# Kernel optimization log

Hardware: AMD Instinct MI355X
Metric: run time of the kernel (lower is better)

Reference implementation:

```python
import jax, jax.numpy as jnp
import numpy as np

H, D, Kd, Vd = 16, 1024, 64, 64
N, Mlen = 4096, 4096


def setup_inputs() -> dict:
    key = jax.random.key(0)
    ks = jax.random.split(key, 7)
    X = jax.random.normal(ks[0], (N, D), dtype=jnp.float32)
    M = jax.random.normal(ks[1], (Mlen, D), dtype=jnp.float32)
    mask = jax.random.randint(ks[2], (N, Mlen), 0, 2, dtype=jnp.int32)
    Wq = jax.random.normal(ks[3], (H, D, Kd), dtype=jnp.float32)
    Wk = jax.random.normal(ks[4], (H, D, Kd), dtype=jnp.float32)
    Wv = jax.random.normal(ks[5], (H, D, Vd), dtype=jnp.float32)
    Wo = jax.random.normal(ks[6], (H, Vd, D), dtype=jnp.float32)
    return {"X": X, "M": M, "mask": mask, "Wq": Wq, "Wk": Wk, "Wv": Wv, "Wo": Wo}


def reference(X, M, mask, Wq, Wk, Wv, Wo):
    # Projections: [h,n,k], [h,m,k], [h,m,v]
    Q = jnp.einsum('nd,hdk->hnk', X, Wq)
    K = jnp.einsum('md,hdk->hmk', M, Wk)
    V = jnp.einsum('md,hdv->hmv', M, Wv)
    # Masked attention (no scaling, matching the source)
    logits = jnp.einsum('hnk,hmk->hnm', Q, K)
    logits = jnp.where(mask[None, :, :] == 0, -jnp.inf, logits)
    weights = jax.nn.softmax(logits, axis=-1)
    O = jnp.einsum('hnm,hmv->hnv', weights, V)
    Y = jnp.einsum('hnv,hvd->nd', O, Wo)
    return Y
```

## Files before the change

kernel.cpp:

```cpp
#include <hip/hip_runtime.h>

typedef _Float16 half8 __attribute__((ext_vector_type(8)));
typedef _Float16 half4 __attribute__((ext_vector_type(4)));
typedef __fp16 fp16x2 __attribute__((ext_vector_type(2)));
typedef short short8 __attribute__((ext_vector_type(8)));
typedef short short4v __attribute__((ext_vector_type(4)));
typedef float floatx4 __attribute__((ext_vector_type(4)));

#define LOG2E 1.4426950408889634f

#define GLDS16(g, l) __builtin_amdgcn_global_load_lds( \
    (const __attribute__((address_space(1))) unsigned int*)(g), \
    (__attribute__((address_space(3))) unsigned int*)(l), 16, 0, 0)

static __device__ __forceinline__ short f2bf(float f){
  union { float f; unsigned u; } v; v.f = f;
  unsigned r = v.u + 0x7fffu + ((v.u >> 16) & 1u);
  return (short)(r >> 16);
}
static __device__ __forceinline__ float bf2f(short s){
  union { unsigned u; float f; } v; v.u = ((unsigned)(unsigned short)s) << 16;
  return v.f;
}

__global__ __launch_bounds__(256) void kconvA(const float* __restrict__ X,
                                              const float* __restrict__ Mm,
                                              short* __restrict__ XFh, short* __restrict__ XFl,
                                              short* __restrict__ MFh, short* __restrict__ MFl){
  int b = blockIdx.x;
  int t = threadIdx.x, w = t >> 6, l = t & 63, quad = l >> 4;
  int srcsel = b >> 8, ntile = b & 255;
  const float* A = srcsel ? Mm : X;
  short* oh = srcsel ? MFh : XFh;
  short* ol = srcsel ? MFl : XFl;
  int row = ntile*16 + (l & 15);
  #pragma unroll
  for (int i = 0; i < 8; i++){
    int kt = w*8 + i;
    const float* p = A + (size_t)row*1024 + kt*32 + quad*8;
    float4 v0 = *(const float4*)p, v1 = *(const float4*)(p + 4);
    float vv[8] = {v0.x,v0.y,v0.z,v0.w,v1.x,v1.y,v1.z,v1.w};
    short8 hh, ll;
    #pragma unroll
    for (int j = 0; j < 8; j++){
      short hb = f2bf(vv[j]); hh[j] = hb; ll[j] = f2bf(vv[j] - bf2f(hb));
    }
    size_t off = ((size_t)kt*256 + ntile)*512 + l*8;
    *(short8*)&oh[off] = hh;
    *(short8*)&ol[off] = ll;
  }
}

__global__ __launch_bounds__(256) void kconvW2(const float* __restrict__ Wq,
                                               const float* __restrict__ Wk,
                                               const float* __restrict__ Wv,
                                               short* __restrict__ WFh, short* __restrict__ WFl){
  __shared__ float T[128][68];
  int bidx = blockIdx.x, g = blockIdx.y;
  int mat = bidx >> 4, h = bidx & 15;
  const float* W = (mat == 0 ? Wq : (mat == 1 ? Wk : Wv)) + (size_t)h*65536;
  int t = threadIdx.x, w = t >> 6, l = t & 63, quad = (l >> 4) & 3, fl = l & 15;
  #pragma unroll
  for (int p = 0; p < 32; p++){
    int idx = p*256 + t, row = idx >> 6, col = idx & 63;
    T[row][col] = W[(size_t)(g*128 + row)*64 + col];
  }
  __syncthreads();
  for (int ktl = 0; ktl < 4; ktl++){
    short8 hh, ll;
    #pragma unroll
    for (int j = 0; j < 8; j++){
      float v = T[ktl*32 + quad*8 + j][w*16 + fl];
      short hb = f2bf(v); hh[j] = hb; ll[j] = f2bf(v - bf2f(hb));
    }
    size_t frag = ((size_t)bidx*32 + g*4 + ktl)*4 + w;
    *(short8*)&WFh[frag*512 + l*8] = hh;
    *(short8*)&WFl[frag*512 + l*8] = ll;
  }
}

__global__ __launch_bounds__(256) void kmaskpack(const int* __restrict__ mask,
                                                 unsigned* __restrict__ bits){
  int w = blockIdx.x * 256 + threadIdx.x;
  const int* p = mask + (size_t)w * 32;
  unsigned b = 0;
  #pragma unroll
  for (int i = 0; i < 32; i++) b |= (p[i] != 0) ? (1u << i) : 0u;
  bits[w] = b;
}

__global__ __launch_bounds__(256) void ktransw(const float* __restrict__ src,
                                               short* __restrict__ dsth,
                                               short* __restrict__ dstl,
                                               int R, int C){
  __shared__ float tile[32][33];
  size_t boff = (size_t)blockIdx.z * R * C;
  src += boff; dsth += boff; dstl += boff;
  int r0 = blockIdx.y*32, c0 = blockIdx.x*32;
  int t = threadIdx.x, tr = t >> 3, tc = (t & 7)*4;
  const float* s = src + (size_t)(r0 + tr)*C + c0 + tc;
  #pragma unroll
  for (int i = 0; i < 4; i++) tile[tr][tc + i] = s[i];
  __syncthreads();
  short* dh = dsth + (size_t)(c0 + tr)*R + r0 + tc;
  short* dl = dstl + (size_t)(c0 + tr)*R + r0 + tc;
  #pragma unroll
  for (int i = 0; i < 4; i++){
    float v = tile[tc + i][tr];
    short hb = f2bf(v);
    dh[i] = hb; dl[i] = f2bf(v - bf2f(hb));
  }
}

__global__ __launch_bounds__(256,2) void kproj2(
    const short* __restrict__ XFh, const short* __restrict__ XFl,
    const short* __restrict__ MFh, const short* __restrict__ MFl,
    const short* __restrict__ WFh, const short* __restrict__ WFl,
    _Float16* __restrict__ QFh, _Float16* __restrict__ QFl,
    _Float16* __restrict__ KFh, _Float16* __restrict__ KFl,
    _Float16* __restrict__ VF)
{
  __shared__ short AhL[4096], AlL[4096], BhL[2048], BlL[2048];
  int cb = blockIdx.x, rb = blockIdx.y;
  int mat = cb >> 4, h = cb & 15;
  const short* Ah = (mat == 0) ? XFh : MFh;
  const short* Al = (mat == 0) ? XFl : MFl;
  int t = threadIdx.x, w = t >> 6, l = t & 63, quad = l >> 4, ln = l & 15;
  floatx4 acc[2][4] = {};
  for (int kt = 0; kt < 32; kt++){
    __syncthreads();
    size_t abase = ((size_t)kt*256 + rb*8)*512;
    #pragma unroll
    for (int i = 0; i < 2; i++){
      int cidx = i*256 + t;
      GLDS16(Ah + abase + cidx*8, &AhL[(i*256 + w*64)*8]);
      GLDS16(Al + abase + cidx*8, &AlL[(i*256 + w*64)*8]);
    }
    size_t bbase = (((size_t)cb*32 + kt)*4)*512;
    GLDS16(WFh + bbase + t*8, &BhL[(w*64)*8]);
    GLDS16(WFl + bbase + t*8, &BlL[(w*64)*8]);
    __syncthreads();
    short8 bh[4], bl[4];
    #pragma unroll
    for (int nt = 0; nt < 4; nt++){
      bh[nt] = *(short8*)&BhL[nt*512 + l*8];
      bl[nt] = *(short8*)&BlL[nt*512 + l*8];
    }
    #pragma unroll
    for (int mt = 0; mt < 2; mt++){
      short8 ah = *(short8*)&AhL[(w*2 + mt)*512 + l*8];
      short8 al = *(short8*)&AlL[(w*2 + mt)*512 + l*8];
      #pragma unroll
      for (int nt = 0; nt < 4; nt++){
        acc[mt][nt] = __builtin_amdgcn_mfma_f32_16x16x32_bf16(ah, bh[nt], acc[mt][nt], 0, 0, 0);
        acc[mt][nt] = __builtin_amdgcn_mfma_f32_16x16x32_bf16(ah, bl[nt], acc[mt][nt], 0, 0, 0);
        acc[mt][nt] = __builtin_amdgcn_mfma_f32_16x16x32_bf16(al, bh[nt], acc[mt][nt], 0, 0, 0);
      }
    }
  }
  int row0 = rb*128;
  if (mat == 2){
    #pragma unroll
    for (int mt = 0; mt < 2; mt++)
      #pragma unroll
      for (int nt = 0; nt < 4; nt++){
        union { fp16x2 h2[2]; unsigned u2[2]; } pu;
        pu.h2[0] = __builtin_amdgcn_cvt_pkrtz(acc[mt][nt][0], acc[mt][nt][1]);
        pu.h2[1] = __builtin_amdgcn_cvt_pkrtz(acc[mt][nt][2], acc[mt][nt][3]);
        size_t base = (((size_t)h*32 + rb)*16 + nt*4 + w)*512;
        *(uint2*)&VF[base + (quad*16 + ln)*8 + mt*4] = *(uint2*)&pu.u2[0];
      }
  } else {
    #pragma unroll
    for (int mt = 0; mt < 2; mt++)
      #pragma unroll
      for (int nt = 0; nt < 4; nt++)
        #pragma unroll
        for (int rg = 0; rg < 4; rg++){
          int n = row0 + w*32 + mt*16 + quad*4 + rg;
          int c = nt*16 + ln;
          float v = acc[mt][nt][rg];
          if (mat == 0) v *= LOG2E;
          _Float16 hi = (_Float16)v;
          _Float16 lo = (_Float16)(v - (float)hi);
          int lane2 = (n & 15) + (((c >> 3) & 3) << 4);
          size_t off = (((size_t)h*256 + (n >> 4))*2 + (c >> 5))*512 + lane2*8 + (c & 7);
          if (mat == 0){ QFh[off] = hi; QFl[off] = lo; }
          else         { KFh[off] = hi; KFl[off] = lo; }
        }
  }
}

__global__ __launch_bounds__(256,4) void kattn7(
    const _Float16* __restrict__ QFh, const _Float16* __restrict__ QFl,
    const _Float16* __restrict__ KFh, const _Float16* __restrict__ KFl,
    const _Float16* __restrict__ VF, const unsigned* __restrict__ bits,
    short* __restrict__ Ows)
{
  __shared__ _Float16 KBh[2][4096], KBl[2][4096], VB[4096];
  int bx = blockIdx.x, h = bx & 15, qb = bx >> 4, q0 = qb*64;
  int t = threadIdx.x, w = t >> 6, l = t & 63, quad = l >> 4, ln = l & 15;

  half8 qh[2], ql[2];
  #pragma unroll
  for (int kc = 0; kc < 2; kc++){
    size_t off = (((size_t)h*256 + qb*4 + w)*2 + kc)*512 + l*8;
    qh[kc] = *(const half8*)&QFh[off];
    ql[kc] = *(const half8*)&QFl[off];
  }

  floatx4 o[4] = {};
  float mst = -1e30f, lst = 0.f;

  const size_t hb = (size_t)h*262144;
  const int cidx0 = t, cidx1 = 256 + t;
  const int ld0 = (w*64)*8, ld1 = (256 + w*64)*8;

  {
    GLDS16(KFh + hb + cidx0*8, &KBh[0][ld0]);
    GLDS16(KFh + hb + cidx1*8, &KBh[0][ld1]);
    GLDS16(KFl + hb + cidx0*8, &KBl[0][ld0]);
    GLDS16(KFl + hb + cidx1*8, &KBl[0][ld1]);
    #pragma unroll
    for (int i = 0; i < 2; i++){
      int cidx = i*256 + t;
      int lu = cidx >> 6, uoff = (cidx & 63)*8;
      int gu = (lu >> 1)*4 + (lu & 1);
      GLDS16(VF + hb + (size_t)gu*512 + uoff, &VB[(i*256 + w*64)*8]);
    }
  }
  uint2 mwv = *(const uint2*)&bits[(size_t)(q0 + w*16 + ln)*128];
  __syncthreads();

  int cur = 0;
  for (int kt = 0; kt < 64; kt++){
    int ktn = (kt + 1) & 63;
    size_t kbn = hb + (size_t)ktn*4096;
    GLDS16(KFh + kbn + cidx0*8, &KBh[cur^1][ld0]);
    GLDS16(KFh + kbn + cidx1*8, &KBh[cur^1][ld1]);
    GLDS16(KFl + kbn + cidx0*8, &KBl[cur^1][ld0]);
    GLDS16(KFl + kbn + cidx1*8, &KBl[cur^1][ld1]);
    uint2 mwn = *(const uint2*)&bits[(size_t)(q0 + w*16 + ln)*128 + ktn*2];

    floatx4 st[4] = {};
    #pragma unroll
    for (int kc = 0; kc < 2; kc++)
      #pragma unroll
      for (int m8 = 0; m8 < 4; m8++){
        half8 kh = *(half8*)&KBh[cur][(m8*2 + kc)*512 + l*8];
        half8 kl = *(half8*)&KBl[cur][(m8*2 + kc)*512 + l*8];
        st[m8] = __builtin_amdgcn_mfma_f32_16x16x32_f16(kh, qh[kc], st[m8], 0, 0, 0);
        st[m8] = __builtin_amdgcn_mfma_f32_16x16x32_f16(kl, qh[kc], st[m8], 0, 0, 0);
        st[m8] = __builtin_amdgcn_mfma_f32_16x16x32_f16(kh, ql[kc], st[m8], 0, 0, 0);
      }

    {
      const unsigned mwp[2] = {mwv.x, mwv.y};
      #pragma unroll
      for (int m8 = 0; m8 < 4; m8++){
        unsigned nib = (mwp[m8 >> 1] >> ((m8 & 1)*16 + quad*4)) & 15u;
        #pragma unroll
        for (int rg = 0; rg < 4; rg++)
          if (!((nib >> rg) & 1u)) st[m8][rg] = -1e30f;
      }
      float a0 = fmaxf(fmaxf(st[0][0], st[0][1]), fmaxf(st[0][2], st[0][3]));
      float a1 = fmaxf(fmaxf(st[1][0], st[1][1]), fmaxf(st[1][2], st[1][3]));
      float a2 = fmaxf(fmaxf(st[2][0], st[2][1]), fmaxf(st[2][2], st[2][3]));
      float a3 = fmaxf(fmaxf(st[3][0], st[3][1]), fmaxf(st[3][2], st[3][3]));
      float mx = fmaxf(fmaxf(a0, a1), fmaxf(a2, a3));
      mx = fmaxf(mx, __shfl_xor(mx, 16));
      mx = fmaxf(mx, __shfl_xor(mx, 32));
      if (__any(mx > mst + 8.0f)){
        float mnew = fmaxf(mst, mx);
        float alpha = exp2f(mst - mnew);
        mst = mnew;
        lst *= alpha;
        #pragma unroll
        for (int vt = 0; vt < 4; vt++) o[vt] *= alpha;
      }
      float ssum = 0.f;
      #pragma unroll
      for (int m8 = 0; m8 < 4; m8++)
        #pragma unroll
        for (int rg = 0; rg < 4; rg++){
          float p = exp2f(st[m8][rg] - mst);
          st[m8][rg] = p; ssum += p;
        }
      ssum += __shfl_xor(ssum, 16);
      ssum += __shfl_xor(ssum, 32);
      lst += ssum;
    }
    mwv = mwn;

    __syncthreads();

    #pragma unroll
    for (int p = 0; p < 2; p++){
      half8 vfp[4];
      #pragma unroll
      for (int vt = 0; vt < 4; vt++)
        vfp[vt] = *(half8*)&VB[((vt*2 + p)*512) + l*8];
      #pragma unroll
      for (int sub = 0; sub < 2; sub++){
        int m8 = p*2 + sub;
        union { fp16x2 h2[2]; half4 h4; } pu;
        pu.h2[0] = __builtin_amdgcn_cvt_pkrtz(st[m8][0], st[m8][1]);
        pu.h2[1] = __builtin_amdgcn_cvt_pkrtz(st[m8][2], st[m8][3]);
        #pragma unroll
        for (int vt = 0; vt < 4; vt++){
          half4 va = sub ? __builtin_shufflevector(vfp[vt], vfp[vt], 4,5,6,7)
                         : __builtin_shufflevector(vfp[vt], vfp[vt], 0,1,2,3);
          o[vt] = __builtin_amdgcn_mfma_f32_16x16x16f16(va, pu.h4, o[vt], 0, 0, 0);
        }
      }
    }

    __syncthreads();

    {
      size_t vbn = hb + (size_t)(ktn >> 1)*8192;
      int vhalf = (ktn & 1)*2;
      #pragma unroll
      for (int i = 0; i < 2; i++){
        int cidx = i*256 + t;
        int lu = cidx >> 6, uoff = (cidx & 63)*8;
        int gu = (lu >> 1)*4 + vhalf + (lu & 1);
        GLDS16(VF + vbn + (size_t)gu*512 + uoff, &VB[(i*256 + w*64)*8]);
      }
    }
    cur ^= 1;
  }

  {
    float inv = (lst > 0.f) ? (1.f / lst) : 0.f;
    int n = q0 + w*16 + ln;
    #pragma unroll
    for (int vt = 0; vt < 4; vt++){
      short4v pk;
      #pragma unroll
      for (int rg = 0; rg < 4; rg++) pk[rg] = f2bf(o[vt][rg]*inv);
      *(short4v*)&Ows[(size_t)n*1024 + h*64 + vt*16 + quad*4] = pk;
    }
  }
}

__global__ __launch_bounds__(256,2) void kfinal(const short* __restrict__ Ain,
                                                const short* __restrict__ Bt,
                                                float* __restrict__ Y)
{
  __shared__ short Al[128*48];
  __shared__ short Bl[64*48];
  int cb = blockIdx.x, rb = blockIdx.y;
  int row0 = rb*128, col0 = cb*64;
  int t = threadIdx.x, w = t >> 6, l = t & 63, quad = l >> 4, ln = l & 15;
  floatx4 acc[2][4] = {};
  for (int d0 = 0; d0 < 1024; d0 += 32){
    #pragma unroll
    for (int i = 0; i < 2; i++){
      int u = t + i*256, r = u >> 2, s = u & 3;
      *(int4*)&Al[r*48 + s*8] = *(const int4*)&Ain[(size_t)(row0 + r)*1024 + d0 + s*8];
    }
    { int r = t >> 2, s = t & 3;
      *(int4*)&Bl[r*48 + s*8] = *(const int4*)&Bt[(size_t)(col0 + r)*1024 + d0 + s*8]; }
    __syncthreads();
    short8 bf[4];
    #pragma unroll
    for (int nt = 0; nt < 4; nt++) bf[nt] = *(short8*)&Bl[(nt*16 + ln)*48 + quad*8];
    #pragma unroll
    for (int mt = 0; mt < 2; mt++){
      short8 af = *(short8*)&Al[(w*32 + mt*16 + ln)*48 + quad*8];
      #pragma unroll
      for (int nt = 0; nt < 4; nt++)
        acc[mt][nt] = __builtin_amdgcn_mfma_f32_16x16x32_bf16(af, bf[nt], acc[mt][nt], 0, 0, 0);
    }
    __syncthreads();
  }
  #pragma unroll
  for (int mt = 0; mt < 2; mt++)
    #pragma unroll
    for (int nt = 0; nt < 4; nt++)
      #pragma unroll
      for (int rg = 0; rg < 4; rg++){
        int n = row0 + w*32 + mt*16 + quad*4 + rg;
        int c = col0 + nt*16 + ln;
        Y[(size_t)n*1024 + c] = acc[mt][nt][rg];
      }
}

extern "C" void kernel_launch(void* const* d_in, const int* in_sizes, int n_in,
                              void* d_out, int out_size, void* d_ws, size_t ws_size,
                              hipStream_t stream){
  (void)in_sizes; (void)n_in; (void)out_size; (void)ws_size;
  const float* X    = (const float*)d_in[0];
  const float* Mm   = (const float*)d_in[1];
  const int*   mask = (const int*)d_in[2];
  const float* Wq   = (const float*)d_in[3];
  const float* Wk   = (const float*)d_in[4];
  const float* Wv   = (const float*)d_in[5];
  const float* Wo   = (const float*)d_in[6];
  float* Y = (float*)d_out;
  char* ws = (char*)d_ws;
  const size_t MB = 1024*1024;
  short*    XFh   = (short*)   (ws +  0*MB);
  short*    XFl   = (short*)   (ws +  8*MB);
  short*    MFh   = (short*)   (ws + 16*MB);
  short*    MFl   = (short*)   (ws + 24*MB);
  short*    WFh   = (short*)   (ws + 32*MB);
  short*    WFl   = (short*)   (ws + 38*MB);
  unsigned* bits  = (unsigned*)(ws + 44*MB);
  _Float16* QFh   = (_Float16*)(ws + 46*MB);
  _Float16* QFl   = (_Float16*)(ws + 54*MB);
  _Float16* KFh   = (_Float16*)(ws + 62*MB);
  _Float16* KFl   = (_Float16*)(ws + 70*MB);
  _Float16* VF    = (_Float16*)(ws + 78*MB);
  short*    Ows   = (short*)   (ws +  0*MB);
  short*    Wot   = (short*)   (ws +  8*MB);
  short*    Wotl  = (short*)   (ws + 10*MB);

  kconvA<<<512, 256, 0, stream>>>(X, Mm, XFh, XFl, MFh, MFl);
  kconvW2<<<dim3(48,8), 256, 0, stream>>>(Wq, Wk, Wv, WFh, WFl);
  kmaskpack<<<2048, 256, 0, stream>>>(mask, bits);
  kproj2<<<dim3(48,32), 256, 0, stream>>>(XFh, XFl, MFh, MFl, WFh, WFl,
                                          QFh, QFl, KFh, KFl, VF);
  ktransw<<<dim3(32,32,1), 256, 0, stream>>>(Wo, Wot, Wotl, 1024, 1024);
  kattn7<<<1024, 256, 0, stream>>>(QFh, QFl, KFh, KFl, VF, bits, Ows);
  kfinal<<<dim3(16,32), 256, 0, stream>>>(Ows, Wot, Y);
}
```

Before: 489.2 us.

## Fuse K and V projections sharing M tiles; raise MFMA priority in attention

The projection kernel now computes K and V in one block, loading each M tile once and running two weight sets against it. The grid shrinks from 48 to 32 column blocks, and the occupancy hint changes from 2 to 3. The attention kernel wraps its MFMA phases in s_setprio to favour matrix issue across waves. It also defers the cross-lane reduction of the softmax denominator to the end of the loop instead of doing it every tile. The costs are more accumulator registers and LDS in the fused blocks, and uneven work between Q blocks and K/V blocks.

```diff
diff --git a/kernel.cpp b/kernel.cpp
--- a/kernel.cpp
+++ b/kernel.cpp
@@ -112,7 +112,7 @@
   }
 }
 
-__global__ __launch_bounds__(256,2) void kproj2(
+__global__ __launch_bounds__(256,3) void kproj3(
     const short* __restrict__ XFh, const short* __restrict__ XFl,
     const short* __restrict__ MFh, const short* __restrict__ MFl,
     const short* __restrict__ WFh, const short* __restrict__ WFl,
@@ -120,13 +120,14 @@
     _Float16* __restrict__ KFh, _Float16* __restrict__ KFl,
     _Float16* __restrict__ VF)
 {
-  __shared__ short AhL[4096], AlL[4096], BhL[2048], BlL[2048];
+  __shared__ short AhL[4096], AlL[4096], BhL[4096], BlL[4096];
   int cb = blockIdx.x, rb = blockIdx.y;
-  int mat = cb >> 4, h = cb & 15;
-  const short* Ah = (mat == 0) ? XFh : MFh;
-  const short* Al = (mat == 0) ? XFl : MFl;
+  const bool fused = (cb >= 16);
+  int h = fused ? (cb - 16) : cb;
+  const short* Ah = fused ? MFh : XFh;
+  const short* Al = fused ? MFl : XFl;
   int t = threadIdx.x, w = t >> 6, l = t & 63, quad = l >> 4, ln = l & 15;
-  floatx4 acc[2][4] = {};
+  floatx4 acc[2][8] = {};
   for (int kt = 0; kt < 32; kt++){
     __syncthreads();
     size_t abase = ((size_t)kt*256 + rb*8)*512;
@@ -136,40 +137,71 @@
       GLDS16(Ah + abase + cidx*8, &AhL[(i*256 + w*64)*8]);
       GLDS16(Al + abase + cidx*8, &AlL[(i*256 + w*64)*8]);
     }
-    size_t bbase = (((size_t)cb*32 + kt)*4)*512;
-    GLDS16(WFh + bbase + t*8, &BhL[(w*64)*8]);
-    GLDS16(WFl + bbase + t*8, &BlL[(w*64)*8]);
-    __syncthreads();
-    short8 bh[4], bl[4];
-    #pragma unroll
-    for (int nt = 0; nt < 4; nt++){
-      bh[nt] = *(short8*)&BhL[nt*512 + l*8];
-      bl[nt] = *(short8*)&BlL[nt*512 + l*8];
-    }
+    size_t bb0 = (((size_t)cb*32 + kt)*4)*512;
+    GLDS16(WFh + bb0 + t*8, &BhL[(w*64)*8]);
+    GLDS16(WFl + bb0 + t*8, &BlL[(w*64)*8]);
+    if (fused){
+      size_t bb1 = (((size_t)(cb + 16)*32 + kt)*4)*512;
+      GLDS16(WFh + bb1 + t*8, &BhL[(256 + w*64)*8]);
+      GLDS16(WFl + bb1 + t*8, &BlL[(256 + w*64)*8]);
+    }
+    __syncthreads();
+    short8 ah[2], al[2];
     #pragma unroll
     for (int mt = 0; mt < 2; mt++){
-      short8 ah = *(short8*)&AhL[(w*2 + mt)*512 + l*8];
-      short8 al = *(short8*)&AlL[(w*2 + mt)*512 + l*8];
+      ah[mt] = *(short8*)&AhL[(w*2 + mt)*512 + l*8];
+      al[mt] = *(short8*)&AlL[(w*2 + mt)*512 + l*8];
+    }
+    {
+      short8 bh[4], bl[4];
       #pragma unroll
       for (int nt = 0; nt < 4; nt++){
-        acc[mt][nt] = __builtin_amdgcn_mfma_f32_16x16x32_bf16(ah, bh[nt], acc[mt][nt], 0, 0, 0);
-        acc[mt][nt] = __builtin_amdgcn_mfma_f32_16x16x32_bf16(ah, bl[nt], acc[mt][nt], 0, 0, 0);
-        acc[mt][nt] = __builtin_amdgcn_mfma_f32_16x16x32_bf16(al, bh[nt], acc[mt][nt], 0, 0, 0);
-      }
+        bh[nt] = *(short8*)&BhL[nt*512 + l*8];
+        bl[nt] = *(short8*)&BlL[nt*512 + l*8];
+      }
+      #pragma unroll
+      for (int mt = 0; mt < 2; mt++)
+        #pragma unroll
+        for (int nt = 0; nt < 4; nt++){
+          acc[mt][nt] = __builtin_amdgcn_mfma_f32_16x16x32_bf16(ah[mt], bh[nt], acc[mt][nt], 0, 0, 0);
+          acc[mt][nt] = __builtin_amdgcn_mfma_f32_16x16x32_bf16(ah[mt], bl[nt], acc[mt][nt], 0, 0, 0);
+          acc[mt][nt] = __builtin_amdgcn_mfma_f32_16x16x32_bf16(al[mt], bh[nt], acc[mt][nt], 0, 0, 0);
+        }
+    }
+    if (fused){
+      short8 bh[4], bl[4];
+      #pragma unroll
+      for (int nt = 0; nt < 4; nt++){
+        bh[nt] = *(short8*)&BhL[(4 + nt)*512 + l*8];
+        bl[nt] = *(short8*)&BlL[(4 + nt)*512 + l*8];
+      }
+      #pragma unroll
+      for (int mt = 0; mt < 2; mt++)
+        #pragma unroll
+        for (int nt = 0; nt < 4; nt++){
+          acc[mt][4+nt] = __builtin_amdgcn_mfma_f32_16x16x32_bf16(ah[mt], bh[nt], acc[mt][4+nt], 0, 0, 0);
+          acc[mt][4+nt] = __builtin_amdgcn_mfma_f32_16x16x32_bf16(ah[mt], bl[nt], acc[mt][4+nt], 0, 0, 0);
+          acc[mt][4+nt] = __builtin_amdgcn_mfma_f32_16x16x32_bf16(al[mt], bh[nt], acc[mt][4+nt], 0, 0, 0);
+        }
     }
   }
   int row0 = rb*128;
-  if (mat == 2){
+  if (!fused){
     #pragma unroll
     for (int mt = 0; mt < 2; mt++)
       #pragma unroll
-      for (int nt = 0; nt < 4; nt++){
-        union { fp16x2 h2[2]; unsigned u2[2]; } pu;
-        pu.h2[0] = __builtin_amdgcn_cvt_pkrtz(acc[mt][nt][0], acc[mt][nt][1]);
-        pu.h2[1] = __builtin_amdgcn_cvt_pkrtz(acc[mt][nt][2], acc[mt][nt][3]);
-        size_t base = (((size_t)h*32 + rb)*16 + nt*4 + w)*512;
-        *(uint2*)&VF[base + (quad*16 + ln)*8 + mt*4] = *(uint2*)&pu.u2[0];
-      }
+      for (int nt = 0; nt < 4; nt++)
+        #pragma unroll
+        for (int rg = 0; rg < 4; rg++){
+          int n = row0 + w*32 + mt*16 + quad*4 + rg;
+          int c = nt*16 + ln;
+          float v = acc[mt][nt][rg] * LOG2E;
+          _Float16 hi = (_Float16)v;
+          _Float16 lo = (_Float16)(v - (float)hi);
+          int lane2 = (n & 15) + (((c >> 3) & 3) << 4);
+          size_t off = (((size_t)h*256 + (n >> 4))*2 + (c >> 5))*512 + lane2*8 + (c & 7);
+          QFh[off] = hi; QFl[off] = lo;
+        }
   } else {
     #pragma unroll
     for (int mt = 0; mt < 2; mt++)
@@ -180,18 +212,26 @@
           int n = row0 + w*32 + mt*16 + quad*4 + rg;
           int c = nt*16 + ln;
           float v = acc[mt][nt][rg];
-          if (mat == 0) v *= LOG2E;
           _Float16 hi = (_Float16)v;
           _Float16 lo = (_Float16)(v - (float)hi);
           int lane2 = (n & 15) + (((c >> 3) & 3) << 4);
           size_t off = (((size_t)h*256 + (n >> 4))*2 + (c >> 5))*512 + lane2*8 + (c & 7);
-          if (mat == 0){ QFh[off] = hi; QFl[off] = lo; }
-          else         { KFh[off] = hi; KFl[off] = lo; }
-        }
-  }
-}
-
-__global__ __launch_bounds__(256,4) void kattn7(
+          KFh[off] = hi; KFl[off] = lo;
+        }
+    #pragma unroll
+    for (int mt = 0; mt < 2; mt++)
+      #pragma unroll
+      for (int ntv = 0; ntv < 4; ntv++){
+        union { fp16x2 h2[2]; unsigned u2[2]; } pu;
+        pu.h2[0] = __builtin_amdgcn_cvt_pkrtz(acc[mt][4+ntv][0], acc[mt][4+ntv][1]);
+        pu.h2[1] = __builtin_amdgcn_cvt_pkrtz(acc[mt][4+ntv][2], acc[mt][4+ntv][3]);
+        size_t base = (((size_t)h*32 + rb)*16 + ntv*4 + w)*512;
+        *(uint2*)&VF[base + (quad*16 + ln)*8 + mt*4] = *(uint2*)&pu.u2[0];
+      }
+  }
+}
+
+__global__ __launch_bounds__(256,4) void kattn8(
     const _Float16* __restrict__ QFh, const _Float16* __restrict__ QFl,
     const _Float16* __restrict__ KFh, const _Float16* __restrict__ KFl,
     const _Float16* __restrict__ VF, const unsigned* __restrict__ bits,
@@ -243,6 +283,7 @@
     uint2 mwn = *(const uint2*)&bits[(size_t)(q0 + w*16 + ln)*128 + ktn*2];
 
     floatx4 st[4] = {};
+    __builtin_amdgcn_s_setprio(1);
     #pragma unroll
     for (int kc = 0; kc < 2; kc++)
       #pragma unroll
@@ -253,6 +294,7 @@
         st[m8] = __builtin_amdgcn_mfma_f32_16x16x32_f16(kl, qh[kc], st[m8], 0, 0, 0);
         st[m8] = __builtin_amdgcn_mfma_f32_16x16x32_f16(kh, ql[kc], st[m8], 0, 0, 0);
       }
+    __builtin_amdgcn_s_setprio(0);
 
     {
       const unsigned mwp[2] = {mwv.x, mwv.y};
@@ -286,14 +328,13 @@
           float p = exp2f(st[m8][rg] - mst);
           st[m8][rg] = p; ssum += p;
         }
-      ssum += __shfl_xor(ssum, 16);
-      ssum += __shfl_xor(ssum, 32);
       lst += ssum;
     }
     mwv = mwn;
 
     __syncthreads();
 
+    __builtin_amdgcn_s_setprio(1);
     #pragma unroll
     for (int p = 0; p < 2; p++){
       half8 vfp[4];
@@ -314,6 +355,7 @@
         }
       }
     }
+    __builtin_amdgcn_s_setprio(0);
 
     __syncthreads();
 
@@ -332,6 +374,8 @@
   }
 
   {
+    lst += __shfl_xor(lst, 16);
+    lst += __shfl_xor(lst, 32);
     float inv = (lst > 0.f) ? (1.f / lst) : 0.f;
     int n = q0 + w*16 + ln;
     #pragma unroll
@@ -420,9 +464,9 @@
   kconvA<<<512, 256, 0, stream>>>(X, Mm, XFh, XFl, MFh, MFl);
   kconvW2<<<dim3(48,8), 256, 0, stream>>>(Wq, Wk, Wv, WFh, WFl);
   kmaskpack<<<2048, 256, 0, stream>>>(mask, bits);
-  kproj2<<<dim3(48,32), 256, 0, stream>>>(XFh, XFl, MFh, MFl, WFh, WFl,
+  kproj3<<<dim3(32,32), 256, 0, stream>>>(XFh, XFl, MFh, MFl, WFh, WFl,
                                           QFh, QFl, KFh, KFl, VF);
   ktransw<<<dim3(32,32,1), 256, 0, stream>>>(Wo, Wot, Wotl, 1024, 1024);
-  kattn7<<<1024, 256, 0, stream>>>(QFh, QFl, KFh, KFl, VF, bits, Ows);
+  kattn8<<<1024, 256, 0, stream>>>(QFh, QFl, KFh, KFl, VF, bits, Ows);
   kfinal<<<dim3(16,32), 256, 0, stream>>>(Ows, Wot, Y);
 }
```

After: 459.0 us. 6.2% less time.
